# Performance work log

Measured on AMD Instinct MI355X. Metric: run time of the kernel, lower is better.

The kernel has to match this reference:

```python
import jax, jax.numpy as jnp
import numpy as np

N = 50000
E = 800000
D = 128
EPS = 1e-5


def setup_inputs() -> dict:
    key = jax.random.key(0)
    ks = jax.random.split(key, 12)
    s1 = 1.0 / np.sqrt(2 * D)
    s2 = 1.0 / np.sqrt(D)
    return {
        "x": jax.random.normal(ks[0], (N, D), dtype=jnp.float32),
        "edge_index": jax.random.randint(ks[1], (2, E), 0, N, dtype=jnp.int32),
        # message MLP: Linear(2D->D), SiLU, Linear(D->D)
        "wm1": jax.random.uniform(ks[2], (2 * D, D), jnp.float32, -s1, s1),
        "bm1": jax.random.uniform(ks[3], (D,), jnp.float32, -s1, s1),
        "wm2": jax.random.uniform(ks[4], (D, D), jnp.float32, -s2, s2),
        "bm2": jax.random.uniform(ks[5], (D,), jnp.float32, -s2, s2),
        # update MLP: Linear(2D->D), SiLU, Linear(D->D)
        "wu1": jax.random.uniform(ks[6], (2 * D, D), jnp.float32, -s1, s1),
        "bu1": jax.random.uniform(ks[7], (D,), jnp.float32, -s1, s1),
        "wu2": jax.random.uniform(ks[8], (D, D), jnp.float32, -s2, s2),
        "bu2": jax.random.uniform(ks[9], (D,), jnp.float32, -s2, s2),
        # LayerNorm affine
        "gamma": jnp.ones((D,), jnp.float32),
        "beta": jnp.zeros((D,), jnp.float32),
    }


def reference(x, edge_index, wm1, bm1, wm2, bm2, wu1, bu1, wu2, bu2, gamma, beta):
    row, col = edge_index[0], edge_index[1]
    # gather endpoints and build message input [E, 2D]
    msg_in = jnp.concatenate([x[row], x[col]], axis=-1)
    h = jax.nn.silu(msg_in @ wm1 + bm1)
    messages = h @ wm2 + bm2  # [E, D]
    # scatter-add aggregate into destination rows
    aggr = jax.ops.segment_sum(messages, row, num_segments=x.shape[0])  # [N, D]
    upd_in = jnp.concatenate([x, aggr], axis=-1)  # [N, 2D]
    u = jax.nn.silu(upd_in @ wu1 + bu1)
    out = u @ wu2 + bu2  # [N, D]
    # residual + LayerNorm
    y = x + out
    mu = jnp.mean(y, axis=-1, keepdims=True)
    var = jnp.var(y, axis=-1, keepdims=True)
    yn = (y - mu) * jax.lax.rsqrt(var + EPS)
    return yn * gamma + beta
```

## Files before the change

kernel.cpp:

```cpp
#include <hip/hip_runtime.h>
#include <hip/hip_bf16.h>

#define NN 50000
#define EE 800000
#define DD 128
#define TILES (EE / 64)
#define NB_SCAN ((NN + 255) / 256)
#define HIST_BLKS ((EE + 255) / 256)
#define FRAG_BLKS 384
#define PQ_BLKS ((NN + 63) / 64)

typedef __attribute__((ext_vector_type(8))) short bf8v;
typedef __attribute__((ext_vector_type(4))) float f4v;
typedef __attribute__((ext_vector_type(4))) unsigned int u4v;

static __device__ __forceinline__ unsigned int bpack2(float lo, float hi) {
    union { __hip_bfloat162 h2; unsigned int u; } c;
    c.h2 = __float22bfloat162_rn(float2{lo, hi});
    return c.u;
}
static __device__ __forceinline__ u4v pack8(f4v a, f4v b) {
    u4v r;
    r[0] = bpack2(a[0], a[1]); r[1] = bpack2(a[2], a[3]);
    r[2] = bpack2(b[0], b[1]); r[3] = bpack2(b[2], b[3]);
    return r;
}
static __device__ __forceinline__ short f2bf_s(float f) {
    union { __hip_bfloat16 h; short s; } c;
    c.h = __float2bfloat16(f);
    return c.s;
}
static __device__ __forceinline__ float bf_lo(unsigned int u) {
    union { unsigned int u; float f; } c; c.u = u << 16; return c.f;
}
static __device__ __forceinline__ float bf_hi(unsigned int u) {
    union { unsigned int u; float f; } c; c.u = u & 0xffff0000u; return c.f;
}
static __device__ __forceinline__ float silu(float v) {
    return v * __builtin_amdgcn_rcpf(1.f + __expf(-v));
}

__global__ __launch_bounds__(256) void mega1_kernel(
    const int* __restrict__ ei, int* __restrict__ cnt, int* __restrict__ rank, int do_sort,
    const float* __restrict__ wm1, const float* __restrict__ wm2,
    const float* __restrict__ wu1, const float* __restrict__ wu2,
    short* __restrict__ wf, float* __restrict__ aggr)
{
    int b = blockIdx.x;
    if (b < HIST_BLKS) {
        if (do_sort) {
            int e = b * 256 + threadIdx.x;
            if (e < EE) rank[e] = atomicAdd(&cnt[ei[e]], 1);
        }
        return;
    }
    int idx = (b - HIST_BLKS) * 256 + threadIdx.x;
    {
        const float* src; int l;
        if      (idx < 32768) { src = wm1; l = idx; }
        else if (idx < 49152) { src = wm2; l = idx - 32768; }
        else if (idx < 81920) { src = wu1; l = idx - 49152; }
        else                  { src = wu2; l = idx - 81920; }
        int e    = l & 7;
        int lane = (l >> 3) & 63;
        int ntg  = (l >> 9) & 7;
        int kc   = l >> 12;
        wf[idx] = f2bf_s(src[(kc * 32 + (lane >> 4) * 8 + e) * DD + ntg * 16 + (lane & 15)]);
    }
    f4v z = (f4v){0.f, 0.f, 0.f, 0.f};
    for (int i = idx; i < NN * DD / 4; i += FRAG_BLKS * 256) ((f4v*)aggr)[i] = z;
}

__global__ __launch_bounds__(256) void scanA_kernel(const int* __restrict__ cnt,
                                                    int* __restrict__ bsum) {
    __shared__ int sd[256];
    int t = threadIdx.x;
    int i = blockIdx.x * 256 + t;
    sd[t] = (i < NN) ? cnt[i] : 0;
    __syncthreads();
    for (int off = 128; off > 0; off >>= 1) {
        if (t < off) sd[t] += sd[t + off];
        __syncthreads();
    }
    if (t == 0) bsum[blockIdx.x] = sd[0];
}

__global__ __launch_bounds__(256) void scanC2_kernel(const int* __restrict__ cnt,
                                                     const int* __restrict__ bsum,
                                                     int* __restrict__ cursor,
                                                     unsigned short* __restrict__ rows16) {
    __shared__ int sb[256];
    __shared__ int sd[256];
    int t = threadIdx.x;
    sb[t] = (t < NB_SCAN) ? bsum[t] : 0;
    __syncthreads();
    for (int off = 1; off < 256; off <<= 1) {
        int u = (t >= off) ? sb[t - off] : 0;
        __syncthreads();
        sb[t] += u;
        __syncthreads();
    }
    int blockpre = (blockIdx.x == 0) ? 0 : sb[blockIdx.x - 1];
    __syncthreads();
    int i = blockIdx.x * 256 + t;
    int v = (i < NN) ? cnt[i] : 0;
    sd[t] = v;
    __syncthreads();
    for (int off = 1; off < 256; off <<= 1) {
        int u = (t >= off) ? sd[t - off] : 0;
        __syncthreads();
        sd[t] += u;
        __syncthreads();
    }
    if (i < NN) {
        int c0 = blockpre + sd[t] - v;
        cursor[i] = c0;
        for (int k = 0; k < v; ++k) rows16[c0 + k] = (unsigned short)i;
    }
}

__global__ __launch_bounds__(256) void mega2_kernel(
    const int* __restrict__ ei, const int* __restrict__ cursor, const int* __restrict__ rank,
    unsigned short* __restrict__ srtc16, int do_sort,
    const float* __restrict__ x, const short* __restrict__ W1f, const float* __restrict__ bm1,
    short* __restrict__ P, short* __restrict__ Q)
{
    __shared__ char smem[32768];
    int b = blockIdx.x;
    if (b < HIST_BLKS) {
        if (do_sort) {
            int e = b * 256 + threadIdx.x;
            if (e < EE) srtc16[cursor[ei[e]] + rank[e]] = (unsigned short)ei[EE + e];
        }
        return;
    }
    const int tid = threadIdx.x;
    const int w = tid >> 6, lane = tid & 63;
    const int rbase = (b - HIST_BLKS) * 64;
    const int rloc = tid >> 2, s = tid & 3;

    {
        int rg = rbase + rloc;
        int rgc = rg < NN ? rg : NN - 1;
        const float* xr = x + (size_t)rgc * DD + s * 32;
        int swz = (rloc & 7) << 4;
        #pragma unroll
        for (int j = 0; j < 4; ++j) {
            f4v a0 = *(const f4v*)(xr + j * 8);
            f4v a1 = *(const f4v*)(xr + j * 8 + 4);
            *(u4v*)(smem + ((rloc * 256 + s * 64 + j * 16) ^ swz)) = pack8(a0, a1);
        }
    }

    bf8v w1t[4][2], w1b[4][2];
    #pragma unroll
    for (int kc = 0; kc < 4; ++kc)
        #pragma unroll
        for (int nt = 0; nt < 2; ++nt) {
            w1t[kc][nt] = *(const bf8v*)(W1f + (((kc * 8) + (w * 2 + nt)) * 64 + lane) * 8);
            w1b[kc][nt] = *(const bf8v*)(W1f + ((((kc + 4) * 8) + (w * 2 + nt)) * 64 + lane) * 8);
        }
    __syncthreads();

    f4v accP[4][2], accQ[4][2];
    #pragma unroll
    for (int mt = 0; mt < 4; ++mt)
        #pragma unroll
        for (int nt = 0; nt < 2; ++nt) {
            accP[mt][nt] = (f4v){0.f, 0.f, 0.f, 0.f};
            accQ[mt][nt] = (f4v){0.f, 0.f, 0.f, 0.f};
        }
    #pragma unroll
    for (int kc = 0; kc < 4; ++kc) {
        bf8v a[4];
        int kb = kc * 64 + (lane >> 4) * 16;
        #pragma unroll
        for (int mt = 0; mt < 4; ++mt) {
            int row = mt * 16 + (lane & 15);
            a[mt] = *(const bf8v*)(smem + ((row * 256 + kb) ^ ((row & 7) << 4)));
        }
        #pragma unroll
        for (int mt = 0; mt < 4; ++mt)
            #pragma unroll
            for (int nt = 0; nt < 2; ++nt) {
                accP[mt][nt] = __builtin_amdgcn_mfma_f32_16x16x32_bf16(a[mt], w1t[kc][nt], accP[mt][nt], 0, 0, 0);
                accQ[mt][nt] = __builtin_amdgcn_mfma_f32_16x16x32_bf16(a[mt], w1b[kc][nt], accQ[mt][nt], 0, 0, 0);
            }
    }
    __syncthreads();

    int col0 = w * 32 + (lane & 15);
    float b1a = bm1[col0], b1b = bm1[col0 + 16];
    #pragma unroll
    for (int mt = 0; mt < 4; ++mt)
        #pragma unroll
        for (int nt = 0; nt < 2; ++nt) {
            float bb = nt ? b1b : b1a;
            int col = col0 + nt * 16;
            #pragma unroll
            for (int r = 0; r < 4; ++r) {
                int row = mt * 16 + (lane >> 4) * 4 + r;
                int off = (row * 256 + col * 2) ^ ((row & 7) << 4);
                *(short*)(smem + off)         = f2bf_s(accP[mt][nt][r] + bb);
                *(short*)(smem + 16384 + off) = f2bf_s(accQ[mt][nt][r]);
            }
        }
    __syncthreads();

    {
        int rg = rbase + rloc;
        if (rg < NN) {
            int swz = (rloc & 7) << 4;
            #pragma unroll
            for (int j = 0; j < 4; ++j) {
                int off = (rloc * 256 + s * 64 + j * 16) ^ swz;
                *(u4v*)(P + (size_t)rg * DD + s * 32 + j * 8) = *(const u4v*)(smem + off);
                *(u4v*)(Q + (size_t)rg * DD + s * 32 + j * 8) = *(const u4v*)(smem + 16384 + off);
            }
        }
    }
}

__global__ __launch_bounds__(256, 8) void edge_kernel(
    const short* __restrict__ P, const short* __restrict__ Q,
    const unsigned short* __restrict__ rows16, const unsigned short* __restrict__ srtc16,
    const int* __restrict__ ei, int use_sorted,
    const short* __restrict__ W2f, const float* __restrict__ bm2,
    float* __restrict__ aggr)
{
    __shared__ char smem[16384 + 256];
    char* Hs = smem;
    int* rows_s = (int*)(smem + 16384);

    const int tid = threadIdx.x;
    const int w = tid >> 6, lane = tid & 63;
    const int rloc = tid >> 2, s = tid & 3;

    {
        int eg = blockIdx.x * 64 + rloc;
        int r, c;
        if (use_sorted) { r = rows16[eg]; c = srtc16[eg]; }
        else            { r = ei[eg];     c = ei[EE + eg]; }
        if (s == 0) rows_s[rloc] = r;
        const u4v* pr = (const u4v*)(P + (size_t)r * DD + s * 32);
        const u4v* qr = (const u4v*)(Q + (size_t)c * DD + s * 32);
        int swz = (rloc & 7) << 4;
        #pragma unroll
        for (int j = 0; j < 4; ++j) {
            u4v pj = pr[j], qj = qr[j];
            u4v hv;
            #pragma unroll
            for (int k2 = 0; k2 < 4; ++k2) {
                float lo = silu(bf_lo(pj[k2]) + bf_lo(qj[k2]));
                float hi = silu(bf_hi(pj[k2]) + bf_hi(qj[k2]));
                hv[k2] = bpack2(lo, hi);
            }
            *(u4v*)(Hs + ((rloc * 256 + s * 64 + j * 16) ^ swz)) = hv;
        }
    }

    bf8v w2f[4][2];
    #pragma unroll
    for (int kc = 0; kc < 4; ++kc)
        #pragma unroll
        for (int nt = 0; nt < 2; ++nt)
            w2f[kc][nt] = *(const bf8v*)(W2f + (((kc * 8) + (w * 2 + nt)) * 64 + lane) * 8);
    int col0 = w * 32 + (lane & 15);
    float b2a = bm2[col0], b2b = bm2[col0 + 16];

    __syncthreads();

    f4v acc2[4][2];
    #pragma unroll
    for (int mt = 0; mt < 4; ++mt)
        #pragma unroll
        for (int nt = 0; nt < 2; ++nt)
            acc2[mt][nt] = (f4v){0.f, 0.f, 0.f, 0.f};
    #pragma unroll
    for (int kc = 0; kc < 4; ++kc) {
        bf8v a[4];
        int kb = kc * 64 + (lane >> 4) * 16;
        #pragma unroll
        for (int mt = 0; mt < 4; ++mt) {
            int row = mt * 16 + (lane & 15);
            a[mt] = *(const bf8v*)(Hs + ((row * 256 + kb) ^ ((row & 7) << 4)));
        }
        #pragma unroll
        for (int mt = 0; mt < 4; ++mt)
            #pragma unroll
            for (int nt = 0; nt < 2; ++nt)
                acc2[mt][nt] = __builtin_amdgcn_mfma_f32_16x16x32_bf16(a[mt], w2f[kc][nt], acc2[mt][nt], 0, 0, 0);
    }
    __syncthreads();

    #pragma unroll
    for (int mt = 0; mt < 4; ++mt)
        #pragma unroll
        for (int nt = 0; nt < 2; ++nt) {
            int col = col0 + nt * 16;
            float bb = nt ? b2b : b2a;
            #pragma unroll
            for (int r = 0; r < 4; ++r) {
                int row = mt * 16 + (lane >> 4) * 4 + r;
                *(short*)(Hs + ((row * 256 + col * 2) ^ ((row & 7) << 4))) = f2bf_s(acc2[mt][nt][r] + bb);
            }
        }
    __syncthreads();

    {
        int col = tid & 127;
        int r0 = (tid >> 7) * 32;
        int cur = rows_s[r0];
        float run = 0.f;
        for (int k = 0; k < 32; ++k) {
            int row = r0 + k;
            int d = rows_s[row];
            unsigned short sv = *(const unsigned short*)(Hs + ((row * 256 + col * 2) ^ ((row & 7) << 4)));
            union { unsigned int u; float f; } c; c.u = ((unsigned int)sv) << 16;
            if (d != cur) {
                unsafeAtomicAdd(aggr + (size_t)cur * DD + col, run);
                run = 0.f; cur = d;
            }
            run += c.f;
        }
        unsafeAtomicAdd(aggr + (size_t)cur * DD + col, run);
    }
}

__global__ __launch_bounds__(256, 4) void node_kernel(
    const float* __restrict__ x, const float* __restrict__ aggr,
    const short* __restrict__ U1f, const short* __restrict__ U2f,
    const float* __restrict__ bu1, const float* __restrict__ bu2,
    const float* __restrict__ gmm, const float* __restrict__ bta,
    float* __restrict__ out)
{
    __shared__ char smem[64 * 512 + 2048];
    char* As = smem;
    float* ps  = (float*)(smem + 64 * 512);
    float* ps2 = ps + 256;

    const int tid = threadIdx.x;
    const int w = tid >> 6, lane = tid & 63;
    const int rbase = blockIdx.x * 64;
    const int rloc = tid >> 2, s = tid & 3;

    {
        int rg = rbase + rloc;
        int rgc = rg < NN ? rg : 0;
        const float* xr = x + (size_t)rgc * DD + s * 32;
        const float* ar = aggr + (size_t)rgc * DD + s * 32;
        int swz = (rloc & 7) << 4;
        #pragma unroll
        for (int i2 = 0; i2 < 4; ++i2) {
            f4v a0 = *(const f4v*)(xr + i2 * 8);
            f4v a1 = *(const f4v*)(xr + i2 * 8 + 4);
            int addr = rloc * 512 + s * 64 + i2 * 16;
            *(u4v*)(As + (addr ^ swz)) = pack8(a0, a1);
            f4v b0 = *(const f4v*)(ar + i2 * 8);
            f4v b1 = *(const f4v*)(ar + i2 * 8 + 4);
            int addr2 = rloc * 512 + 256 + s * 64 + i2 * 16;
            *(u4v*)(As + (addr2 ^ swz)) = pack8(b0, b1);
        }
    }

    bf8v u1f[8][2], u2f[4][2];
    #pragma unroll
    for (int kc = 0; kc < 8; ++kc)
        #pragma unroll
        for (int nt = 0; nt < 2; ++nt)
            u1f[kc][nt] = *(const bf8v*)(U1f + (((kc * 8) + (w * 2 + nt)) * 64 + lane) * 8);
    #pragma unroll
    for (int kc = 0; kc < 4; ++kc)
        #pragma unroll
        for (int nt = 0; nt < 2; ++nt)
            u2f[kc][nt] = *(const bf8v*)(U2f + (((kc * 8) + (w * 2 + nt)) * 64 + lane) * 8);

    __syncthreads();

    f4v acc[4][2];
    #pragma unroll
    for (int mt = 0; mt < 4; ++mt)
        #pragma unroll
        for (int nt = 0; nt < 2; ++nt)
            acc[mt][nt] = (f4v){0.f, 0.f, 0.f, 0.f};
    #pragma unroll
    for (int kc = 0; kc < 8; ++kc) {
        bf8v a[4];
        int kb = kc * 64 + (lane >> 4) * 16;
        #pragma unroll
        for (int mt = 0; mt < 4; ++mt) {
            int row = mt * 16 + (lane & 15);
            a[mt] = *(const bf8v*)(As + ((row * 512 + kb) ^ ((row & 7) << 4)));
        }
        #pragma unroll
        for (int mt = 0; mt < 4; ++mt)
            #pragma unroll
            for (int nt = 0; nt < 2; ++nt)
                acc[mt][nt] = __builtin_amdgcn_mfma_f32_16x16x32_bf16(a[mt], u1f[kc][nt], acc[mt][nt], 0, 0, 0);
    }
    __syncthreads();

    int col0 = w * 32 + (lane & 15);
    float b1a = bu1[col0], b1b = bu1[col0 + 16];
    #pragma unroll
    for (int mt = 0; mt < 4; ++mt)
        #pragma unroll
        for (int nt = 0; nt < 2; ++nt) {
            float bb = nt ? b1b : b1a;
            int col = col0 + nt * 16;
            #pragma unroll
            for (int r = 0; r < 4; ++r) {
                float v = silu(acc[mt][nt][r] + bb);
                int row = mt * 16 + (lane >> 4) * 4 + r;
                *(short*)(As + ((row * 256 + col * 2) ^ ((row & 7) << 4))) = f2bf_s(v);
            }
        }
    __syncthreads();

    f4v acc2[4][2];
    #pragma unroll
    for (int mt = 0; mt < 4; ++mt)
        #pragma unroll
        for (int nt = 0; nt < 2; ++nt)
            acc2[mt][nt] = (f4v){0.f, 0.f, 0.f, 0.f};
    #pragma unroll
    for (int kc = 0; kc < 4; ++kc) {
        bf8v a[4];
        int kb = kc * 64 + (lane >> 4) * 16;
        #pragma unroll
        for (int mt = 0; mt < 4; ++mt) {
            int row = mt * 16 + (lane & 15);
            a[mt] = *(const bf8v*)(As + ((row * 256 + kb) ^ ((row & 7) << 4)));
        }
        #pragma unroll
        for (int mt = 0; mt < 4; ++mt)
            #pragma unroll
            for (int nt = 0; nt < 2; ++nt)
                acc2[mt][nt] = __builtin_amdgcn_mfma_f32_16x16x32_bf16(a[mt], u2f[kc][nt], acc2[mt][nt], 0, 0, 0);
    }
    __syncthreads();

    float b2a = bu2[col0], b2b = bu2[col0 + 16];
    #pragma unroll
    for (int mt = 0; mt < 4; ++mt)
        #pragma unroll
        for (int nt = 0; nt < 2; ++nt) {
            int col = col0 + nt * 16;
            float bb = nt ? b2b : b2a;
            #pragma unroll
            for (int r = 0; r < 4; ++r) {
                int rowl = mt * 16 + (lane >> 4) * 4 + r;
                int rg = rbase + rowl;
                int rgc = rg < NN ? rg : 0;
                float xv = x[(size_t)rgc * DD + col];
                float y = acc2[mt][nt][r] + bb + xv;
                *(float*)(As + ((rowl * 512 + col * 4) ^ ((rowl & 7) << 4))) = y;
            }
        }
    __syncthreads();

    {
        int q = tid & 3;
        float s1 = 0.f, s2 = 0.f;
        #pragma unroll
        for (int i = 0; i < 8; ++i) {
            f4v v = *(const f4v*)(As + ((rloc * 512 + q * 128 + i * 16) ^ ((rloc & 7) << 4)));
            s1 += v[0] + v[1] + v[2] + v[3];
            s2 += v[0] * v[0] + v[1] * v[1] + v[2] * v[2] + v[3] * v[3];
        }
        ps[rloc * 4 + q] = s1;
        ps2[rloc * 4 + q] = s2;
    }
    __syncthreads();
    {
        int q = tid & 3;
        float fs  = ps[rloc * 4] + ps[rloc * 4 + 1] + ps[rloc * 4 + 2] + ps[rloc * 4 + 3];
        float fs2 = ps2[rloc * 4] + ps2[rloc * 4 + 1] + ps2[rloc * 4 + 2] + ps2[rloc * 4 + 3];
        float mu  = fs * (1.f / 128.f);
        float var = fs2 * (1.f / 128.f) - mu * mu;
        float inv = rsqrtf(var + 1e-5f);
        int rg = rbase + rloc;
        if (rg < NN) {
            #pragma unroll
            for (int i = 0; i < 8; ++i) {
                int col = q * 32 + i * 4;
                f4v v  = *(const f4v*)(As + ((rloc * 512 + col * 4) ^ ((rloc & 7) << 4)));
                f4v gg = *(const f4v*)(gmm + col);
                f4v bb = *(const f4v*)(bta + col);
                f4v o;
                #pragma unroll
                for (int j = 0; j < 4; ++j)
                    o[j] = (v[j] - mu) * inv * gg[j] + bb[j];
                *(f4v*)(out + (size_t)rg * DD + col) = o;
            }
        }
    }
}

extern "C" void kernel_launch(void* const* d_in, const int* in_sizes, int n_in,
                              void* d_out, int out_size, void* d_ws, size_t ws_size,
                              hipStream_t stream) {
    const float* x    = (const float*)d_in[0];
    const int*   ei   = (const int*)d_in[1];
    const float* wm1  = (const float*)d_in[2];
    const float* bm1  = (const float*)d_in[3];
    const float* wm2  = (const float*)d_in[4];
    const float* bm2  = (const float*)d_in[5];
    const float* wu1  = (const float*)d_in[6];
    const float* bu1  = (const float*)d_in[7];
    const float* wu2  = (const float*)d_in[8];
    const float* bu2  = (const float*)d_in[9];
    const float* gmm  = (const float*)d_in[10];
    const float* bta  = (const float*)d_in[11];
    float* out = (float*)d_out;

    const size_t off_P      = 0;
    const size_t off_Q      = 12800000;
    const size_t off_frags  = 25600000;
    const size_t off_cnt    = 25796608;
    const size_t off_cur    = 25996608;
    const size_t off_bsum   = 26196608;
    const size_t off_rows16 = 26197632;
    const size_t off_srtc16 = 27797632;
    const size_t off_rank   = 29397632;
    const size_t need_sort  = 32597632;

    char* wsB = (char*)d_ws;
    short* P    = (short*)(wsB + off_P);
    short* Q    = (short*)(wsB + off_Q);
    short* Wf   = (short*)(wsB + off_frags);
    short* W1f  = Wf;
    short* W2f  = Wf + 32768;
    short* U1f  = Wf + 49152;
    short* U2f  = Wf + 81920;
    int*   cnt    = (int*)(wsB + off_cnt);
    int*   cursor = (int*)(wsB + off_cur);
    int*   bsum   = (int*)(wsB + off_bsum);
    unsigned short* rows16 = (unsigned short*)(wsB + off_rows16);
    unsigned short* srtc16 = (unsigned short*)(wsB + off_srtc16);
    int*   rank   = (int*)(wsB + off_rank);

    float* aggr = (float*)d_out;

    int do_sort = (ws_size >= need_sort) ? 1 : 0;

    hipMemsetAsync(cnt, 0, (size_t)NN * 4, stream);
    mega1_kernel<<<HIST_BLKS + FRAG_BLKS, 256, 0, stream>>>(
        ei, cnt, rank, do_sort, wm1, wm2, wu1, wu2, Wf, aggr);

    if (do_sort) {
        scanA_kernel<<<NB_SCAN, 256, 0, stream>>>(cnt, bsum);
        scanC2_kernel<<<NB_SCAN, 256, 0, stream>>>(cnt, bsum, cursor, rows16);
    }
    mega2_kernel<<<HIST_BLKS + PQ_BLKS, 256, 0, stream>>>(
        ei, cursor, rank, srtc16, do_sort, x, W1f, bm1, P, Q);

    edge_kernel<<<TILES, 256, 0, stream>>>(P, Q, rows16, srtc16, ei, do_sort, W2f, bm2, aggr);
    node_kernel<<<(NN + 63) / 64, 256, 0, stream>>>(x, aggr, U1f, U2f, bu1, bu2, gmm, bta, out);
}
```

Before: 191.9 us.

## Bucket edges by destination block and accumulate aggregates in shared memory

```diff
diff --git a/kernel.cpp b/kernel.cpp
--- a/kernel.cpp
+++ b/kernel.cpp
@@ -9,6 +9,8 @@
 #define HIST_BLKS ((EE + 255) / 256)
 #define FRAG_BLKS 384
 #define PQ_BLKS ((NN + 63) / 64)
+#define DB 32
+#define NB_EDGE ((NN + DB - 1) / DB)
 
 typedef __attribute__((ext_vector_type(8))) short bf8v;
 typedef __attribute__((ext_vector_type(4))) float f4v;
@@ -116,6 +118,7 @@
         int c0 = blockpre + sd[t] - v;
         cursor[i] = c0;
         for (int k = 0; k < v; ++k) rows16[c0 + k] = (unsigned short)i;
+        if (i == NN - 1) cursor[NN] = c0 + v;
     }
 }
 
@@ -221,10 +224,147 @@
     }
 }
 
-__global__ __launch_bounds__(256, 8) void edge_kernel(
+__global__ __launch_bounds__(256, 4) void edge_bucket_kernel(
     const short* __restrict__ P, const short* __restrict__ Q,
     const unsigned short* __restrict__ rows16, const unsigned short* __restrict__ srtc16,
-    const int* __restrict__ ei, int use_sorted,
+    const int* __restrict__ cursor, const int* __restrict__ cnt,
+    const short* __restrict__ W2f, const float* __restrict__ bm2,
+    float* __restrict__ aggr)
+{
+    __shared__ char tileB[DB * DD * 4];
+    __shared__ char HsB[64 * 256];
+    __shared__ short drow_s[64];
+
+    const int tid = threadIdx.x;
+    const int w = tid >> 6, lane = tid & 63;
+    const int rloc = tid >> 2, s = tid & 3;
+    const int d0 = blockIdx.x * DB;
+
+    {
+        f4v z = (f4v){0.f, 0.f, 0.f, 0.f};
+        int swz = ((tid >> 3) & 7) << 4;
+        #pragma unroll
+        for (int i = 0; i < 4; ++i)
+            *(f4v*)(tileB + ((tid * 64 + i * 16) ^ swz)) = z;
+    }
+
+    int hi = d0 + DB; if (hi > NN) hi = NN;
+    const int estart = cursor[d0];
+    const int eend   = cursor[hi];
+
+    bf8v w2f[4][2];
+    #pragma unroll
+    for (int kc = 0; kc < 4; ++kc)
+        #pragma unroll
+        for (int nt = 0; nt < 2; ++nt)
+            w2f[kc][nt] = *(const bf8v*)(W2f + (((kc * 8) + (w * 2 + nt)) * 64 + lane) * 8);
+    const int col0 = w * 32 + (lane & 15);
+
+    __syncthreads();
+
+    for (int e0 = estart; e0 < eend; e0 += 64) {
+        {
+            int eg = e0 + rloc;
+            bool act = eg < eend;
+            int swz = (rloc & 7) << 4;
+            if (act) {
+                int r = rows16[eg];
+                int c = srtc16[eg];
+                if (s == 0) drow_s[rloc] = (short)(r - d0);
+                const u4v* pr = (const u4v*)(P + (size_t)r * DD + s * 32);
+                const u4v* qr = (const u4v*)(Q + (size_t)c * DD + s * 32);
+                #pragma unroll
+                for (int j = 0; j < 4; ++j) {
+                    u4v pj = pr[j], qj = qr[j];
+                    u4v hv;
+                    #pragma unroll
+                    for (int k2 = 0; k2 < 4; ++k2) {
+                        float lo = silu(bf_lo(pj[k2]) + bf_lo(qj[k2]));
+                        float hic = silu(bf_hi(pj[k2]) + bf_hi(qj[k2]));
+                        hv[k2] = bpack2(lo, hic);
+                    }
+                    *(u4v*)(HsB + ((rloc * 256 + s * 64 + j * 16) ^ swz)) = hv;
+                }
+            } else {
+                if (s == 0) drow_s[rloc] = 0;
+                u4v z = (u4v){0u, 0u, 0u, 0u};
+                #pragma unroll
+                for (int j = 0; j < 4; ++j)
+                    *(u4v*)(HsB + ((rloc * 256 + s * 64 + j * 16) ^ swz)) = z;
+            }
+        }
+        __syncthreads();
+
+        f4v acc2[4][2];
+        #pragma unroll
+        for (int mt = 0; mt < 4; ++mt)
+            #pragma unroll
+            for (int nt = 0; nt < 2; ++nt)
+                acc2[mt][nt] = (f4v){0.f, 0.f, 0.f, 0.f};
+        #pragma unroll
+        for (int kc = 0; kc < 4; ++kc) {
+            bf8v a[4];
+            int kb = kc * 64 + (lane >> 4) * 16;
+            #pragma unroll
+            for (int mt = 0; mt < 4; ++mt) {
+                int row = mt * 16 + (lane & 15);
+                a[mt] = *(const bf8v*)(HsB + ((row * 256 + kb) ^ ((row & 7) << 4)));
+            }
+            #pragma unroll
+            for (int mt = 0; mt < 4; ++mt)
+                #pragma unroll
+                for (int nt = 0; nt < 2; ++nt)
+                    acc2[mt][nt] = __builtin_amdgcn_mfma_f32_16x16x32_bf16(a[mt], w2f[kc][nt], acc2[mt][nt], 0, 0, 0);
+        }
+
+        #pragma unroll
+        for (int mt = 0; mt < 4; ++mt) {
+            int bs = mt * 16 + (lane >> 4) * 4;
+            int da = drow_s[bs],     db2 = drow_s[bs + 1];
+            int dc = drow_s[bs + 2], dd2 = drow_s[bs + 3];
+            #pragma unroll
+            for (int nt = 0; nt < 2; ++nt) {
+                int col = col0 + nt * 16;
+                f4v v = acc2[mt][nt];
+                if (da == dd2 && da == db2 && da == dc) {
+                    atomicAdd((float*)(tileB + ((da * 512 + col * 4) ^ ((da & 7) << 4))),
+                              v[0] + v[1] + v[2] + v[3]);
+                } else {
+                    atomicAdd((float*)(tileB + ((da  * 512 + col * 4) ^ ((da  & 7) << 4))), v[0]);
+                    atomicAdd((float*)(tileB + ((db2 * 512 + col * 4) ^ ((db2 & 7) << 4))), v[1]);
+                    atomicAdd((float*)(tileB + ((dc  * 512 + col * 4) ^ ((dc  & 7) << 4))), v[2]);
+                    atomicAdd((float*)(tileB + ((dd2 * 512 + col * 4) ^ ((dd2 & 7) << 4))), v[3]);
+                }
+            }
+        }
+        __syncthreads();
+    }
+
+    {
+        int row = tid >> 3;
+        int scol = (tid & 7) * 16;
+        int node = d0 + row;
+        if (node < NN) {
+            float deg = (float)cnt[node];
+            int swz = (row & 7) << 4;
+            #pragma unroll
+            for (int i = 0; i < 4; ++i) {
+                int col = scol + i * 4;
+                f4v v  = *(const f4v*)(tileB + ((row * 512 + col * 4) ^ swz));
+                f4v bb = *(const f4v*)(bm2 + col);
+                f4v o;
+                #pragma unroll
+                for (int j = 0; j < 4; ++j)
+                    o[j] = v[j] + bb[j] * deg;
+                *(f4v*)(aggr + (size_t)node * DD + col) = o;
+            }
+        }
+    }
+}
+
+__global__ __launch_bounds__(256, 8) void edge_fallback_kernel(
+    const short* __restrict__ P, const short* __restrict__ Q,
+    const int* __restrict__ ei,
     const short* __restrict__ W2f, const float* __restrict__ bm2,
     float* __restrict__ aggr)
 {
@@ -238,9 +378,7 @@
 
     {
         int eg = blockIdx.x * 64 + rloc;
-        int r, c;
-        if (use_sorted) { r = rows16[eg]; c = srtc16[eg]; }
-        else            { r = ei[eg];     c = ei[EE + eg]; }
+        int r = ei[eg], c = ei[EE + eg];
         if (s == 0) rows_s[rloc] = r;
         const u4v* pr = (const u4v*)(P + (size_t)r * DD + s * 32);
         const u4v* qr = (const u4v*)(Q + (size_t)c * DD + s * 32);
@@ -291,7 +429,6 @@
             for (int nt = 0; nt < 2; ++nt)
                 acc2[mt][nt] = __builtin_amdgcn_mfma_f32_16x16x32_bf16(a[mt], w2f[kc][nt], acc2[mt][nt], 0, 0, 0);
     }
-    __syncthreads();
 
     #pragma unroll
     for (int mt = 0; mt < 4; ++mt)
@@ -301,30 +438,10 @@
             float bb = nt ? b2b : b2a;
             #pragma unroll
             for (int r = 0; r < 4; ++r) {
-                int row = mt * 16 + (lane >> 4) * 4 + r;
-                *(short*)(Hs + ((row * 256 + col * 2) ^ ((row & 7) << 4))) = f2bf_s(acc2[mt][nt][r] + bb);
-            }
-        }
-    __syncthreads();
-
-    {
-        int col = tid & 127;
-        int r0 = (tid >> 7) * 32;
-        int cur = rows_s[r0];
-        float run = 0.f;
-        for (int k = 0; k < 32; ++k) {
-            int row = r0 + k;
-            int d = rows_s[row];
-            unsigned short sv = *(const unsigned short*)(Hs + ((row * 256 + col * 2) ^ ((row & 7) << 4)));
-            union { unsigned int u; float f; } c; c.u = ((unsigned int)sv) << 16;
-            if (d != cur) {
-                unsafeAtomicAdd(aggr + (size_t)cur * DD + col, run);
-                run = 0.f; cur = d;
-            }
-            run += c.f;
-        }
-        unsafeAtomicAdd(aggr + (size_t)cur * DD + col, run);
-    }
+                int rowl = mt * 16 + (lane >> 4) * 4 + r;
+                unsafeAtomicAdd(aggr + (size_t)rows_s[rowl] * DD + col, acc2[mt][nt][r] + bb);
+            }
+        }
 }
 
 __global__ __launch_bounds__(256, 4) void node_kernel(
@@ -519,11 +636,11 @@
     const size_t off_frags  = 25600000;
     const size_t off_cnt    = 25796608;
     const size_t off_cur    = 25996608;
-    const size_t off_bsum   = 26196608;
-    const size_t off_rows16 = 26197632;
-    const size_t off_srtc16 = 27797632;
-    const size_t off_rank   = 29397632;
-    const size_t need_sort  = 32597632;
+    const size_t off_bsum   = 26196624;
+    const size_t off_rows16 = 26197648;
+    const size_t off_srtc16 = 27797648;
+    const size_t off_rank   = 29397648;
+    const size_t need_sort  = 32597648;
 
     char* wsB = (char*)d_ws;
     short* P    = (short*)(wsB + off_P);
@@ -555,6 +672,11 @@
     mega2_kernel<<<HIST_BLKS + PQ_BLKS, 256, 0, stream>>>(
         ei, cursor, rank, srtc16, do_sort, x, W1f, bm1, P, Q);
 
-    edge_kernel<<<TILES, 256, 0, stream>>>(P, Q, rows16, srtc16, ei, do_sort, W2f, bm2, aggr);
+    if (do_sort)
+        edge_bucket_kernel<<<NB_EDGE, 256, 0, stream>>>(
+            P, Q, rows16, srtc16, cursor, cnt, W2f, bm2, aggr);
+    else
+        edge_fallback_kernel<<<TILES, 256, 0, stream>>>(P, Q, ei, W2f, bm2, aggr);
+
     node_kernel<<<(NN + 63) / 64, 256, 0, stream>>>(x, aggr, U1f, U2f, bu1, bu2, gmm, bta, out);
 }
```

Result: slower. 403.5 us (+110.3%).
